# Kernel optimization log

Hardware: AMD Instinct MI355X
Metric: run time of the kernel (lower is better)

## Reference

```python
import jax, jax.numpy as jnp
import numpy as np

NUM_FEATURES = 4
LATENT = 16
HIDDEN = 128
N_PIECES = 20
B, P = 8192, 128


def setup_inputs() -> dict:
    key = jax.random.key(0)
    ks = jax.random.split(key, 8)
    s = lambda fan_in: 1.0 / np.sqrt(fan_in)
    return {
        "x": jax.random.normal(ks[0], (B, P * NUM_FEATURES), jnp.float32),
        "W1": jax.random.normal(ks[1], (NUM_FEATURES, HIDDEN), jnp.float32) * s(NUM_FEATURES),
        "b1": jnp.zeros((HIDDEN,), jnp.float32),
        "W2": jax.random.normal(ks[2], (HIDDEN, HIDDEN), jnp.float32) * s(HIDDEN),
        "b2": jnp.zeros((HIDDEN,), jnp.float32),
        "W3": jax.random.normal(ks[3], (HIDDEN, 2 * LATENT), jnp.float32) * s(HIDDEN),
        "b3": jnp.zeros((2 * LATENT,), jnp.float32),
        "pool_weight": jax.random.normal(ks[4], (2 * LATENT, N_PIECES + 1), jnp.float32) * 0.1,
        "eps": jax.random.normal(ks[5], (B, LATENT), jnp.float32),
    }


def _fspool_weights(pool_weight, set_size):
    # piecewise-linear interpolation of pool_weight over normalized rank positions
    pos = jnp.arange(set_size, dtype=jnp.float32) / (set_size - 1) * N_PIECES  # [P]
    idx = jnp.clip(pos.astype(jnp.int32), 0, N_PIECES)
    frac = pos - idx.astype(jnp.float32)
    left = pool_weight[:, idx]                                   # [C, P]
    right = pool_weight[:, jnp.clip(idx + 1, 0, N_PIECES)]       # [C, P]
    return (1.0 - frac) * left + frac * right                    # [C, P]


def reference(x, W1, b1, W2, b2, W3, b3, pool_weight, eps):
    # per-particle shared MLP, batched over particles (B, P, F) -> (B, P, 2L)
    h = x.reshape(B, P, NUM_FEATURES)
    h = jax.nn.relu(jnp.einsum("bpf,fh->bph", h, W1) + b1)
    h = jax.nn.relu(jnp.einsum("bph,hk->bpk", h, W2) + b2)
    h = jnp.einsum("bph,hc->bpc", h, W3) + b3                    # [B, P, 2L]
    z = jnp.transpose(h, (0, 2, 1))                              # [B, 2L, P]
    # FSPool: descending featurewise sort + rank-weighted sum over set dim
    z_sorted = jnp.flip(jnp.sort(z, axis=-1), axis=-1)           # [B, 2L, P]
    w = _fspool_weights(pool_weight, P)                          # [2L, P]
    pooled = jnp.sum(z_sorted * w[None], axis=-1)                # [B, 2L]
    mus = pooled[:, ::2]
    logvars = pooled[:, 1::2]
    samples = mus + eps * jnp.exp(0.5 * logvars)
    return (mus, logvars, samples)
```

## Files before the change

kernel.cpp:

```cpp
#include <hip/hip_runtime.h>

#define B_TOT 8192
#define NB    16
#define NPCS  20

typedef __attribute__((ext_vector_type(8))) __fp16 f16x8;
typedef __attribute__((ext_vector_type(4))) float f32x4;
typedef __attribute__((ext_vector_type(2))) __fp16 fp16x2;

__device__ __forceinline__ unsigned pkmax(unsigned a, unsigned b) {
    unsigned d; asm("v_pk_max_f16 %0, %1, %2" : "=v"(d) : "v"(a), "v"(b)); return d;
}
__device__ __forceinline__ unsigned pkmin(unsigned a, unsigned b) {
    unsigned d; asm("v_pk_min_f16 %0, %1, %2" : "=v"(d) : "v"(a), "v"(b)); return d;
}
__device__ __forceinline__ float h2f(unsigned u) {
    float f; asm("v_cvt_f32_f16 %0, %1" : "=v"(f) : "v"(u)); return f;
}
__device__ __forceinline__ unsigned pkrne(float a, float b) {
    fp16x2 h;
    h.x = (__fp16)a;
    h.y = (__fp16)b;
    return __builtin_bit_cast(unsigned, h);
}
__device__ __forceinline__ float asf(unsigned u) { return __builtin_bit_cast(float, u); }
__device__ __forceinline__ unsigned asu(float f) { return __builtin_bit_cast(unsigned, f); }
__device__ __forceinline__ fp16x2 ash2(unsigned u) { return __builtin_bit_cast(fp16x2, u); }
__device__ __forceinline__ unsigned asu2(fp16x2 h) { return __builtin_bit_cast(unsigned, h); }

template<int CTRL>
__device__ __forceinline__ unsigned dppmov(unsigned v) {
    return (unsigned)__builtin_amdgcn_mov_dpp((int)v, CTRL, 0xf, 0xf, true);
}
__device__ __forceinline__ unsigned xlane(unsigned v, int lm) {
    switch (lm) {
    case 1:  return dppmov<0xB1>(v);
    case 2:  return dppmov<0x4E>(v);
    case 4:  return (unsigned)__builtin_amdgcn_ds_swizzle((int)v, 0x101F);
    default: return dppmov<0x128>(v);
    }
}
__device__ __forceinline__ float xlanef(float v, int lm) { return asf(xlane(asu(v), lm)); }

#define WS_W3T 32768
#define WS_WSP 40960
#define WS_W1D 57344
#define WS_B1D 59392

__device__ __forceinline__ unsigned dup16(float f) {
    unsigned short u = __builtin_bit_cast(unsigned short, (__fp16)f);
    return (unsigned)u * 0x10001u;
}

__global__ void prep_kernel(const float* __restrict__ W1, const float* __restrict__ b1,
                            const float* __restrict__ W2, const float* __restrict__ W3,
                            const float* __restrict__ pw, void* __restrict__ ws)
{
    const int t = blockIdx.x * 256 + threadIdx.x;
    __fp16* w2t = (__fp16*)ws;
    __fp16* w3t = (__fp16*)((char*)ws + WS_W3T);
    float* wsp  = (float*)((char*)ws + WS_WSP);
    unsigned* w1d = (unsigned*)((char*)ws + WS_W1D);
    unsigned* b1d = (unsigned*)((char*)ws + WS_B1D);
    if (t < 16384) {
        int j = t >> 7, k = t & 127;
        w2t[t] = (__fp16)W2[k * 128 + j];
    } else if (t < 20480) {
        int o = t - 16384, c = o >> 7, k = o & 127;
        w3t[o] = (__fp16)W3[k * 32 + c];
    } else if (t < 24576) {
        int o = t - 20480, c = o >> 7, p = o & 127;
        float pos = (float)p * (20.0f / 127.0f);
        int ip = min((int)pos, NPCS);
        float fr = pos - (float)ip;
        int ipb = min(ip + 1, NPCS);
        wsp[o] = (1.0f - fr) * pw[c * 21 + ip] + fr * pw[c * 21 + ipb];
    } else if (t < 24704) {
        int h = t - 24576;
        w1d[h * 4 + 0] = dup16(W1[h]);
        w1d[h * 4 + 1] = dup16(W1[128 + h]);
        w1d[h * 4 + 2] = dup16(W1[256 + h]);
        w1d[h * 4 + 3] = dup16(W1[384 + h]);
        b1d[h] = dup16(b1[h]);
    }
}

#define L_SCR  32768
#define L_SZP  50176
#define L_W1D  58624
#define L_B1D  60672
#define L_POOL 61184

__global__ __launch_bounds__(256, 2) void enc_kernel(
    const float* __restrict__ x,   const float* __restrict__ b1g,
    const float* __restrict__ b2g, const float* __restrict__ b3g,
    const float* __restrict__ eps, const void* __restrict__ ws,
    float* __restrict__ out)
{
    __shared__ __align__(16) char smem[63232];

    const int tid  = threadIdx.x;
    const int wv   = tid >> 6;
    const int lane = tid & 63;
    const int l16  = lane & 15;
    const int quad = lane >> 4;
    const int b0   = blockIdx.x * NB;

    {
        const uint4* src = (const uint4*)ws;
#pragma unroll
        for (int it = 0; it < 8; ++it) {
            int idx = tid + it * 256;
            int j = idx >> 4, ch = idx & 15;
            *(uint4*)(smem + j * 256 + ((ch ^ (j & 15)) * 16)) = src[idx];
        }
    }
    if (tid < 160) ((uint4*)(smem + L_W1D))[tid] = ((const uint4*)((const char*)ws + WS_W1D))[tid];

    f16x8 w3f[2][4];
    {
        const __fp16* w3t = (const __fp16*)((const char*)ws + WS_W3T);
#pragma unroll
        for (int mt2 = 0; mt2 < 2; ++mt2)
#pragma unroll
            for (int kt = 0; kt < 4; ++kt)
                w3f[mt2][kt] = *(const f16x8*)(w3t + (mt2 * 16 + l16) * 128 + kt * 32 + quad * 8);
    }
    float4 b3v[2];
    b3v[0] = *(const float4*)(b3g + quad * 4);
    b3v[1] = *(const float4*)(b3g + 16 + quad * 4);
    float b2r[8];
#pragma unroll
    for (int nt = 0; nt < 8; ++nt) b2r[nt] = b2g[nt * 16 + l16];

    const int pr = wv * 4 + quad;
    float wE[8], wO[8];
    {
        const float* wsp = (const float*)((const char*)ws + WS_WSP);
        float4 e0 = *(const float4*)(wsp + (2 * pr) * 128 + l16 * 8);
        float4 e1 = *(const float4*)(wsp + (2 * pr) * 128 + l16 * 8 + 4);
        float4 o0 = *(const float4*)(wsp + (2 * pr + 1) * 128 + l16 * 8);
        float4 o1 = *(const float4*)(wsp + (2 * pr + 1) * 128 + l16 * 8 + 4);
        wE[0]=e0.x; wE[1]=e0.y; wE[2]=e0.z; wE[3]=e0.w; wE[4]=e1.x; wE[5]=e1.y; wE[6]=e1.z; wE[7]=e1.w;
        wO[0]=o0.x; wO[1]=o0.y; wO[2]=o0.z; wO[3]=o0.w; wO[4]=o1.x; wO[5]=o1.y; wO[6]=o1.z; wO[7]=o1.w;
    }
    __syncthreads();

    __fp16*   scr   = (__fp16*)(smem + L_SCR) + wv * (16 * 136);
    unsigned* szp   = (unsigned*)(smem + L_SZP);
    float*    spool = (float*)(smem + L_POOL);

    const float* xptr = x + (size_t)b0 * 512 + (wv * 32 + l16) * 4;
    float4 xv0 = *(const float4*)(xptr);
    float4 xv1 = *(const float4*)(xptr + 64);

    for (int e = 0; e < NB; ++e) {
        fp16x2 xh[4];
        xh[0].x = (__fp16)xv0.x; xh[0].y = (__fp16)xv1.x;
        xh[1].x = (__fp16)xv0.y; xh[1].y = (__fp16)xv1.y;
        xh[2].x = (__fp16)xv0.z; xh[2].y = (__fp16)xv1.z;
        xh[3].x = (__fp16)xv0.w; xh[3].y = (__fp16)xv1.w;

        if (e + 1 < NB) {
            xv0 = *(const float4*)(xptr + (e + 1) * 512);
            xv1 = *(const float4*)(xptr + (e + 1) * 512 + 64);
        }

        union AF { unsigned u[4]; f16x8 v; } a1[2][4];
#pragma unroll
        for (int kt = 0; kt < 4; ++kt) {
            const int k8 = kt * 32 + quad * 8;
#pragma unroll
            for (int jp = 0; jp < 4; ++jp) {
                const int h = k8 + 2 * jp;
                const uint4 wa = *(const uint4*)(smem + L_W1D + h * 16);
                const uint4 wb = *(const uint4*)(smem + L_W1D + h * 16 + 16);
                const uint2 bp = *(const uint2*)(smem + L_B1D + h * 4);
                fp16x2 accA = ash2(bp.x);
                fp16x2 accB = ash2(bp.y);
                accA = __builtin_elementwise_fma(xh[0], ash2(wa.x), accA);
                accA = __builtin_elementwise_fma(xh[1], ash2(wa.y), accA);
                accA = __builtin_elementwise_fma(xh[2], ash2(wa.z), accA);
                accA = __builtin_elementwise_fma(xh[3], ash2(wa.w), accA);
                accB = __builtin_elementwise_fma(xh[0], ash2(wb.x), accB);
                accB = __builtin_elementwise_fma(xh[1], ash2(wb.y), accB);
                accB = __builtin_elementwise_fma(xh[2], ash2(wb.z), accB);
                accB = __builtin_elementwise_fma(xh[3], ash2(wb.w), accB);
                const unsigned uA = pkmax(asu2(accA), 0u);
                const unsigned uB = pkmax(asu2(accB), 0u);
                a1[0][kt].u[jp] = __builtin_amdgcn_perm(uA, uB, 0x01000504u);
                a1[1][kt].u[jp] = __builtin_amdgcn_perm(uA, uB, 0x03020706u);
            }
        }

        f32x4 acc2[2][8];
#pragma unroll
        for (int mt = 0; mt < 2; ++mt)
#pragma unroll
            for (int nt = 0; nt < 8; ++nt)
                acc2[mt][nt] = (f32x4){b2r[nt], b2r[nt], b2r[nt], b2r[nt]};
#pragma unroll
        for (int kt = 0; kt < 4; ++kt)
#pragma unroll
            for (int nt = 0; nt < 8; ++nt) {
                const int j = nt * 16 + l16;
                const int phys = (kt * 4 + quad) ^ l16;
                f16x8 bf = *(const f16x8*)(smem + j * 256 + phys * 16);
                acc2[0][nt] = __builtin_amdgcn_mfma_f32_16x16x32_f16(a1[0][kt].v, bf, acc2[0][nt], 0, 0, 0);
                acc2[1][nt] = __builtin_amdgcn_mfma_f32_16x16x32_f16(a1[1][kt].v, bf, acc2[1][nt], 0, 0, 0);
            }

#pragma unroll
        for (int mt = 0; mt < 2; ++mt) {
#pragma unroll
            for (int nt = 0; nt < 8; ++nt) {
                const int col = nt * 16 + l16;
#pragma unroll
                for (int r = 0; r < 4; ++r)
                    scr[(quad * 4 + r) * 136 + col] = (__fp16)fmaxf(acc2[mt][nt][r], 0.0f);
            }
            asm volatile("s_waitcnt lgkmcnt(0)" ::: "memory");

            f16x8 a3[4];
#pragma unroll
            for (int kt = 0; kt < 4; ++kt)
                a3[kt] = *(const f16x8*)(scr + l16 * 136 + kt * 32 + quad * 8);

            const int colbase = wv * 32 + mt * 16;
#pragma unroll
            for (int mt2 = 0; mt2 < 2; ++mt2) {
                f32x4 acc = (f32x4){b3v[mt2].x, b3v[mt2].y, b3v[mt2].z, b3v[mt2].w};
#pragma unroll
                for (int kt = 0; kt < 4; ++kt)
                    acc = __builtin_amdgcn_mfma_f32_16x16x32_f16(w3f[mt2][kt], a3[kt], acc, 0, 0, 0);
                const int prw = 8 * mt2 + 2 * quad;
                szp[prw * 132 + colbase + l16]       = pkrne(acc[0], acc[1]);
                szp[(prw + 1) * 132 + colbase + l16] = pkrne(acc[2], acc[3]);
            }
            asm volatile("" ::: "memory");
        }
        __syncthreads();

        unsigned v[8];
        {
            const unsigned* zp = szp + pr * 132 + l16 * 8;
            uint4 za = *(const uint4*)zp;
            uint4 zb = *(const uint4*)(zp + 4);
            v[0]=za.x; v[1]=za.y; v[2]=za.z; v[3]=za.w;
            v[4]=zb.x; v[5]=zb.y; v[6]=zb.z; v[7]=zb.w;
        }
        const int ib = l16 * 8;
#pragma unroll
        for (int k = 2; k <= 128; k <<= 1) {
#pragma unroll
            for (int j = 64; j >= 1; j >>= 1) {
                if (j >= k) continue;
                if (j >= 8) {
                    const bool km = ((ib & k) == 0) != ((ib & j) != 0);
                    const int lm = j >> 3;
#pragma unroll
                    for (int r = 0; r < 8; ++r) {
                        unsigned p = xlane(v[r], lm);
                        unsigned mx = pkmax(v[r], p), mn = pkmin(v[r], p);
                        v[r] = km ? mx : mn;
                    }
                } else if (k <= 4) {
#pragma unroll
                    for (int a = 0; a < 8; ++a) {
                        if (a & j) continue;
                        const int bx = a | j;
                        unsigned mx = pkmax(v[a], v[bx]), mn = pkmin(v[a], v[bx]);
                        if ((a & k) == 0) { v[a] = mx; v[bx] = mn; }
                        else              { v[a] = mn; v[bx] = mx; }
                    }
                } else {
                    const bool km = ((ib & k) == 0);
#pragma unroll
                    for (int a = 0; a < 8; ++a) {
                        if (a & j) continue;
                        const int bx = a | j;
                        unsigned mx = pkmax(v[a], v[bx]), mn = pkmin(v[a], v[bx]);
                        v[a] = km ? mx : mn;
                        v[bx] = km ? mn : mx;
                    }
                }
            }
        }

        float sE = 0.f, sO = 0.f;
#pragma unroll
        for (int r = 0; r < 8; ++r) {
            sE = fmaf(wE[r], h2f(v[r]), sE);
            sO = fmaf(wO[r], h2f(v[r] >> 16), sO);
        }
#pragma unroll
        for (int d = 8; d >= 1; d >>= 1) {
            sE += xlanef(sE, d);
            sO += xlanef(sO, d);
        }
        if (l16 == 0) {
            spool[e * 32 + 2 * pr]     = sE;
            spool[e * 32 + 2 * pr + 1] = sO;
        }
        __syncthreads();
    }

    {
        const int e = tid >> 4, t = tid & 15;
        const float mu = spool[e * 32 + 2 * t];
        const float lv = spool[e * 32 + 2 * t + 1];
        const float ev = eps[(size_t)b0 * 16 + tid];
        const float smp = fmaf(ev, __expf(0.5f * lv), mu);
        out[(size_t)b0 * 16 + tid] = mu;
        out[(size_t)B_TOT * 16 + (size_t)b0 * 16 + tid] = lv;
        out[(size_t)2 * B_TOT * 16 + (size_t)b0 * 16 + tid] = smp;
    }
}

extern "C" void kernel_launch(void* const* d_in, const int* in_sizes, int n_in,
                              void* d_out, int out_size, void* d_ws, size_t ws_size,
                              hipStream_t stream) {
    const float* x   = (const float*)d_in[0];
    const float* W1  = (const float*)d_in[1];
    const float* b1  = (const float*)d_in[2];
    const float* W2  = (const float*)d_in[3];
    const float* b2  = (const float*)d_in[4];
    const float* W3  = (const float*)d_in[5];
    const float* b3  = (const float*)d_in[6];
    const float* pw  = (const float*)d_in[7];
    const float* eps = (const float*)d_in[8];
    float* out = (float*)d_out;

    prep_kernel<<<dim3(97), dim3(256), 0, stream>>>(W1, b1, W2, W3, pw, d_ws);
    enc_kernel<<<dim3(B_TOT / NB), dim3(256), 0, stream>>>(x, b1, b2, b3, eps, d_ws, out);
}
```

Measured before the change: 171.3 us.

## Use transposed packed scratch, sign-flip bitonic stages, and pkrtz conversions

Layer-2 activations are now packed with cvt_pkrtz plus a packed ReLU and written as uint2 into a transposed scratch layout, then gathered back as scalar fp16 reads for the layer-3 MFMA. Within-thread bitonic stages replace per-pair max/min selects with an XOR sign flip before and after each stage, so only one fixed compare direction is needed. Biases are preloaded as MFMA accumulators and x is converted with round-toward-zero. This trims VALU select and conversion work but adds many 16-bit LDS reads and changes rounding of inputs and activations.

```diff
diff --git a/kernel.cpp b/kernel.cpp
--- a/kernel.cpp
+++ b/kernel.cpp
@@ -13,15 +13,15 @@
 }
 __device__ __forceinline__ unsigned pkmin(unsigned a, unsigned b) {
     unsigned d; asm("v_pk_min_f16 %0, %1, %2" : "=v"(d) : "v"(a), "v"(b)); return d;
-}
-__device__ __forceinline__ float h2f(unsigned u) {
-    float f; asm("v_cvt_f32_f16 %0, %1" : "=v"(f) : "v"(u)); return f;
 }
 __device__ __forceinline__ unsigned pkrne(float a, float b) {
     fp16x2 h;
     h.x = (__fp16)a;
     h.y = (__fp16)b;
     return __builtin_bit_cast(unsigned, h);
+}
+__device__ __forceinline__ unsigned pkrtz(float a, float b) {
+    return __builtin_bit_cast(unsigned, __builtin_amdgcn_cvt_pkrtz(a, b));
 }
 __device__ __forceinline__ float asf(unsigned u) { return __builtin_bit_cast(float, u); }
 __device__ __forceinline__ unsigned asu(float f) { return __builtin_bit_cast(unsigned, f); }
@@ -85,11 +85,11 @@
     }
 }
 
-#define L_SCR  32768
-#define L_SZP  50176
-#define L_W1D  58624
-#define L_B1D  60672
-#define L_POOL 61184
+#define L_SCRT 32768
+#define L_SZP  49152
+#define L_W1D  57600
+#define L_B1D  59648
+#define L_POOL 60160
 
 __global__ __launch_bounds__(256, 2) void enc_kernel(
     const float* __restrict__ x,   const float* __restrict__ b1g,
@@ -97,7 +97,7 @@
     const float* __restrict__ eps, const void* __restrict__ ws,
     float* __restrict__ out)
 {
-    __shared__ __align__(16) char smem[63232];
+    __shared__ __align__(16) char smem[62208];
 
     const int tid  = threadIdx.x;
     const int wv   = tid >> 6;
@@ -126,12 +126,19 @@
             for (int kt = 0; kt < 4; ++kt)
                 w3f[mt2][kt] = *(const f16x8*)(w3t + (mt2 * 16 + l16) * 128 + kt * 32 + quad * 8);
     }
-    float4 b3v[2];
-    b3v[0] = *(const float4*)(b3g + quad * 4);
-    b3v[1] = *(const float4*)(b3g + 16 + quad * 4);
-    float b2r[8];
-#pragma unroll
-    for (int nt = 0; nt < 8; ++nt) b2r[nt] = b2g[nt * 16 + l16];
+    f32x4 b3acc[2];
+    {
+        float4 t0 = *(const float4*)(b3g + quad * 4);
+        float4 t1 = *(const float4*)(b3g + 16 + quad * 4);
+        b3acc[0] = (f32x4){t0.x, t0.y, t0.z, t0.w};
+        b3acc[1] = (f32x4){t1.x, t1.y, t1.z, t1.w};
+    }
+    f32x4 b2acc[8];
+#pragma unroll
+    for (int nt = 0; nt < 8; ++nt) {
+        const float bv = b2g[nt * 16 + l16];
+        b2acc[nt] = (f32x4){bv, bv, bv, bv};
+    }
 
     const int pr = wv * 4 + quad;
     float wE[8], wO[8];
@@ -144,9 +151,16 @@
         wE[0]=e0.x; wE[1]=e0.y; wE[2]=e0.z; wE[3]=e0.w; wE[4]=e1.x; wE[5]=e1.y; wE[6]=e1.z; wE[7]=e1.w;
         wO[0]=o0.x; wO[1]=o0.y; wO[2]=o0.z; wO[3]=o0.w; wO[4]=o1.x; wO[5]=o1.y; wO[6]=o1.z; wO[7]=o1.w;
     }
+
+    const int ib = l16 * 8;
+    const unsigned sfl8  = (ib & 8)  ? 0x80008000u : 0u;
+    const unsigned sfl16 = (ib & 16) ? 0x80008000u : 0u;
+    const unsigned sfl32 = (ib & 32) ? 0x80008000u : 0u;
+    const unsigned sfl64 = (ib & 64) ? 0x80008000u : 0u;
+
     __syncthreads();
 
-    __fp16*   scr   = (__fp16*)(smem + L_SCR) + wv * (16 * 136);
+    char*     scrTw = (char*)(smem + L_SCRT + wv * 4096);
     unsigned* szp   = (unsigned*)(smem + L_SZP);
     float*    spool = (float*)(smem + L_POOL);
 
@@ -155,11 +169,10 @@
     float4 xv1 = *(const float4*)(xptr + 64);
 
     for (int e = 0; e < NB; ++e) {
-        fp16x2 xh[4];
-        xh[0].x = (__fp16)xv0.x; xh[0].y = (__fp16)xv1.x;
-        xh[1].x = (__fp16)xv0.y; xh[1].y = (__fp16)xv1.y;
-        xh[2].x = (__fp16)xv0.z; xh[2].y = (__fp16)xv1.z;
-        xh[3].x = (__fp16)xv0.w; xh[3].y = (__fp16)xv1.w;
+        const unsigned xp0 = pkrtz(xv0.x, xv1.x);
+        const unsigned xp1 = pkrtz(xv0.y, xv1.y);
+        const unsigned xp2 = pkrtz(xv0.z, xv1.z);
+        const unsigned xp3 = pkrtz(xv0.w, xv1.w);
 
         if (e + 1 < NB) {
             xv0 = *(const float4*)(xptr + (e + 1) * 512);
@@ -178,14 +191,14 @@
                 const uint2 bp = *(const uint2*)(smem + L_B1D + h * 4);
                 fp16x2 accA = ash2(bp.x);
                 fp16x2 accB = ash2(bp.y);
-                accA = __builtin_elementwise_fma(xh[0], ash2(wa.x), accA);
-                accA = __builtin_elementwise_fma(xh[1], ash2(wa.y), accA);
-                accA = __builtin_elementwise_fma(xh[2], ash2(wa.z), accA);
-                accA = __builtin_elementwise_fma(xh[3], ash2(wa.w), accA);
-                accB = __builtin_elementwise_fma(xh[0], ash2(wb.x), accB);
-                accB = __builtin_elementwise_fma(xh[1], ash2(wb.y), accB);
-                accB = __builtin_elementwise_fma(xh[2], ash2(wb.z), accB);
-                accB = __builtin_elementwise_fma(xh[3], ash2(wb.w), accB);
+                accA = __builtin_elementwise_fma(ash2(xp0), ash2(wa.x), accA);
+                accA = __builtin_elementwise_fma(ash2(xp1), ash2(wa.y), accA);
+                accA = __builtin_elementwise_fma(ash2(xp2), ash2(wa.z), accA);
+                accA = __builtin_elementwise_fma(ash2(xp3), ash2(wa.w), accA);
+                accB = __builtin_elementwise_fma(ash2(xp0), ash2(wb.x), accB);
+                accB = __builtin_elementwise_fma(ash2(xp1), ash2(wb.y), accB);
+                accB = __builtin_elementwise_fma(ash2(xp2), ash2(wb.z), accB);
+                accB = __builtin_elementwise_fma(ash2(xp3), ash2(wb.w), accB);
                 const unsigned uA = pkmax(asu2(accA), 0u);
                 const unsigned uB = pkmax(asu2(accB), 0u);
                 a1[0][kt].u[jp] = __builtin_amdgcn_perm(uA, uB, 0x01000504u);
@@ -195,44 +208,52 @@
 
         f32x4 acc2[2][8];
 #pragma unroll
-        for (int mt = 0; mt < 2; ++mt)
-#pragma unroll
-            for (int nt = 0; nt < 8; ++nt)
-                acc2[mt][nt] = (f32x4){b2r[nt], b2r[nt], b2r[nt], b2r[nt]};
-#pragma unroll
         for (int kt = 0; kt < 4; ++kt)
 #pragma unroll
             for (int nt = 0; nt < 8; ++nt) {
                 const int j = nt * 16 + l16;
                 const int phys = (kt * 4 + quad) ^ l16;
                 f16x8 bf = *(const f16x8*)(smem + j * 256 + phys * 16);
-                acc2[0][nt] = __builtin_amdgcn_mfma_f32_16x16x32_f16(a1[0][kt].v, bf, acc2[0][nt], 0, 0, 0);
-                acc2[1][nt] = __builtin_amdgcn_mfma_f32_16x16x32_f16(a1[1][kt].v, bf, acc2[1][nt], 0, 0, 0);
+                if (kt == 0) {
+                    acc2[0][nt] = __builtin_amdgcn_mfma_f32_16x16x32_f16(a1[0][0].v, bf, b2acc[nt], 0, 0, 0);
+                    acc2[1][nt] = __builtin_amdgcn_mfma_f32_16x16x32_f16(a1[1][0].v, bf, b2acc[nt], 0, 0, 0);
+                } else {
+                    acc2[0][nt] = __builtin_amdgcn_mfma_f32_16x16x32_f16(a1[0][kt].v, bf, acc2[0][nt], 0, 0, 0);
+                    acc2[1][nt] = __builtin_amdgcn_mfma_f32_16x16x32_f16(a1[1][kt].v, bf, acc2[1][nt], 0, 0, 0);
+                }
             }
 
 #pragma unroll
         for (int mt = 0; mt < 2; ++mt) {
 #pragma unroll
             for (int nt = 0; nt < 8; ++nt) {
-                const int col = nt * 16 + l16;
-#pragma unroll
-                for (int r = 0; r < 4; ++r)
-                    scr[(quad * 4 + r) * 136 + col] = (__fp16)fmaxf(acc2[mt][nt][r], 0.0f);
+                const int h = nt * 16 + l16;
+                uint2 pk;
+                pk.x = pkmax(pkrtz(acc2[mt][nt][0], acc2[mt][nt][1]), 0u);
+                pk.y = pkmax(pkrtz(acc2[mt][nt][2], acc2[mt][nt][3]), 0u);
+                *(uint2*)(scrTw + (h >> 2) * 128 + (h & 3) * 32 + quad * 8) = pk;
             }
             asm volatile("s_waitcnt lgkmcnt(0)" ::: "memory");
 
-            f16x8 a3[4];
-#pragma unroll
-            for (int kt = 0; kt < 4; ++kt)
-                a3[kt] = *(const f16x8*)(scr + l16 * 136 + kt * 32 + quad * 8);
+            union A3 { __fp16 h[8]; f16x8 v; } a3[4];
+            {
+                const __fp16* rbase = (const __fp16*)(scrTw + quad * 256) + l16;
+#pragma unroll
+                for (int kt = 0; kt < 4; ++kt) {
+                    const __fp16* rp = rbase + kt * 512;
+#pragma unroll
+                    for (int j = 0; j < 8; ++j)
+                        a3[kt].h[j] = rp[j * 16];
+                }
+            }
 
             const int colbase = wv * 32 + mt * 16;
 #pragma unroll
             for (int mt2 = 0; mt2 < 2; ++mt2) {
-                f32x4 acc = (f32x4){b3v[mt2].x, b3v[mt2].y, b3v[mt2].z, b3v[mt2].w};
-#pragma unroll
-                for (int kt = 0; kt < 4; ++kt)
-                    acc = __builtin_amdgcn_mfma_f32_16x16x32_f16(w3f[mt2][kt], a3[kt], acc, 0, 0, 0);
+                f32x4 acc = __builtin_amdgcn_mfma_f32_16x16x32_f16(w3f[mt2][0], a3[0].v, b3acc[mt2], 0, 0, 0);
+#pragma unroll
+                for (int kt = 1; kt < 4; ++kt)
+                    acc = __builtin_amdgcn_mfma_f32_16x16x32_f16(w3f[mt2][kt], a3[kt].v, acc, 0, 0, 0);
                 const int prw = 8 * mt2 + 2 * quad;
                 szp[prw * 132 + colbase + l16]       = pkrne(acc[0], acc[1]);
                 szp[(prw + 1) * 132 + colbase + l16] = pkrne(acc[2], acc[3]);
@@ -249,7 +270,6 @@
             v[0]=za.x; v[1]=za.y; v[2]=za.z; v[3]=za.w;
             v[4]=zb.x; v[5]=zb.y; v[6]=zb.z; v[7]=zb.w;
         }
-        const int ib = l16 * 8;
 #pragma unroll
         for (int k = 2; k <= 128; k <<= 1) {
 #pragma unroll
@@ -274,14 +294,22 @@
                         else              { v[a] = mn; v[bx] = mx; }
                     }
                 } else {
-                    const bool km = ((ib & k) == 0);
+                    const unsigned sfl = (k == 8) ? sfl8 : (k == 16) ? sfl16 :
+                                         (k == 32) ? sfl32 : (k == 64) ? sfl64 : 0u;
+                    if (j == 4 && k != 128) {
+#pragma unroll
+                        for (int r = 0; r < 8; ++r) v[r] ^= sfl;
+                    }
 #pragma unroll
                     for (int a = 0; a < 8; ++a) {
                         if (a & j) continue;
                         const int bx = a | j;
                         unsigned mx = pkmax(v[a], v[bx]), mn = pkmin(v[a], v[bx]);
-                        v[a] = km ? mx : mn;
-                        v[bx] = km ? mn : mx;
+                        v[a] = mx; v[bx] = mn;
+                    }
+                    if (j == 1 && k != 128) {
+#pragma unroll
+                        for (int r = 0; r < 8; ++r) v[r] ^= sfl;
                     }
                 }
             }
@@ -290,8 +318,9 @@
         float sE = 0.f, sO = 0.f;
 #pragma unroll
         for (int r = 0; r < 8; ++r) {
-            sE = fmaf(wE[r], h2f(v[r]), sE);
-            sO = fmaf(wO[r], h2f(v[r] >> 16), sO);
+            const fp16x2 hv = ash2(v[r]);
+            sE = fmaf(wE[r], (float)hv.x, sE);
+            sO = fmaf(wO[r], (float)hv.y, sO);
         }
 #pragma unroll
         for (int d = 8; d >= 1; d >>= 1) {
```

Result: slower. 180.8 us (+5.5%).
